# Performance work log

Measured on AMD Instinct MI355X. Metric: run time of the kernel, lower is better.

## Reference

```python
import jax, jax.numpy as jnp
import numpy as np

DT = 0.1
DISC = 5  # discretization: time grid arange(0, DT, DT/DISC) -> DISC-1 steps of h=DT/DISC


def setup_inputs() -> dict:
    key = jax.random.key(0)
    ks = jax.random.split(key, 16)
    B, T, D, Z, H = 32, 256, 128, 64, 256
    s = 0.08
    return {
        "x": jax.random.normal(ks[0], (B, T, D), dtype=jnp.float32),
        "h0": jnp.zeros((2, 1, Z), dtype=jnp.float32),
        "Wih0": jax.random.normal(ks[1], (Z, D), dtype=jnp.float32) * s,
        "Whh0": jax.random.normal(ks[2], (Z, Z), dtype=jnp.float32) * s,
        "bih0": jax.random.normal(ks[3], (Z,), dtype=jnp.float32) * s,
        "bhh0": jax.random.normal(ks[4], (Z,), dtype=jnp.float32) * s,
        "Wih1": jax.random.normal(ks[5], (Z, Z), dtype=jnp.float32) * s,
        "Whh1": jax.random.normal(ks[6], (Z, Z), dtype=jnp.float32) * s,
        "bih1": jax.random.normal(ks[7], (Z,), dtype=jnp.float32) * s,
        "bhh1": jax.random.normal(ks[8], (Z,), dtype=jnp.float32) * s,
        "Wh0": jax.random.normal(ks[9], (H, Z), dtype=jnp.float32) * s,
        "bh0": jax.random.normal(ks[10], (H,), dtype=jnp.float32) * s,
        "Wh1": jax.random.normal(ks[11], (H, H), dtype=jnp.float32) * s,
        "bh1": jax.random.normal(ks[12], (H,), dtype=jnp.float32) * s,
        "Wout": jax.random.normal(ks[13], (1, H), dtype=jnp.float32) * s,
        "bout": jax.random.normal(ks[14], (1,), dtype=jnp.float32) * s,
        "seq_len": 256,
    }


def _rnn_layer(xs, h_init, Wih, Whh, bih, bhh):
    # xs: (T, B, in) -> (T, B, Z); tanh RNN (nn.RNN, nonlinearity='tanh')
    def step(h, xt):
        h = jnp.tanh(xt @ Wih.T + bih + h @ Whh.T + bhh)
        return h, h
    _, ys = jax.lax.scan(step, h_init, xs)
    return ys


def _forward(x, h0, Wih0, Whh0, bih0, bhh0, Wih1, Whh1, bih1, bhh1,
             Wh0, bh0, Wh1, bh1, Wout, bout, seq_len):
    B, T, Z = x.shape[0], seq_len, h0.shape[-1]
    # reverse_sequences with full-length sequences == flip along time
    xr = jnp.flip(x, axis=1).transpose(1, 0, 2)  # (T, B, D)
    h0b = jnp.broadcast_to(h0, (2, B, Z))
    y0 = _rnn_layer(xr, h0b[0], Wih0, Whh0, bih0, bhh0)
    y1 = _rnn_layer(y0, h0b[1], Wih1, Whh1, bih1, bhh1)
    rnn_out = jnp.flip(y1.transpose(1, 0, 2), axis=1)  # (B, T, Z), pad_and_reverse

    # Hamiltonian MLP H(z): z_dim -> hidden -> hidden -> 1 (latent_func uses autograd.grad of H)
    def hamiltonian_sum(z):
        h = jnp.tanh(z @ Wh0.T + bh0)
        h = jnp.tanh(h @ Wh1.T + bh1)
        return (h @ Wout.T + bout).sum()
    grad_h = jax.grad(hamiltonian_sum)  # per-sample grads since H is per-sample

    # Yoshida 4th-order symplectic coefficients
    cbrt2 = 2.0 ** (1.0 / 3.0)
    w1 = 1.0 / (2.0 - cbrt2)
    w0 = -cbrt2 * w1
    cs = (w1 / 2.0, (w0 + w1) / 2.0, (w0 + w1) / 2.0, w1 / 2.0)
    ds = (w1, w0, w1)
    h_step = DT / DISC

    def yoshida_step(z, _):
        q, p = jnp.split(z, 2, axis=-1)
        for i in range(4):
            dHq, dHp = jnp.split(grad_h(jnp.concatenate([q, p], -1)), 2, -1)
            q = q + cs[i] * h_step * dHp  # drift: dq/dt = dH/dp
            if i < 3:
                dHq, dHp = jnp.split(grad_h(jnp.concatenate([q, p], -1)), 2, -1)
                p = p - ds[i] * h_step * dHq  # kick: dp/dt = -dH/dq
        return jnp.concatenate([q, p], -1), None

    # ode_output[:, t] = odeint(rnn_out[:, t+1]) for t < T-1; all independent -> batch them
    z0 = rnn_out[:, 1:, :].reshape(B * (T - 1), 2 * (Z // 2))
    zT, _ = jax.lax.scan(yoshida_step, z0, None, length=DISC - 1)
    ode = zT.reshape(B, T - 1, Z)
    return jnp.concatenate([ode, rnn_out[:, -1:, :]], axis=1)  # (B, T, Z)


def reference(x, h0, Wih0, Whh0, bih0, bhh0, Wih1, Whh1, bih1, bhh1,
              Wh0, bh0, Wh1, bh1, Wout, bout, seq_len):
    return _forward(x, h0, Wih0, Whh0, bih0, bhh0, Wih1, Whh1, bih1, bhh1,
                    Wh0, bh0, Wh1, bh1, Wout, bout, seq_len)
```

## Files before the change

kernel.cpp:

```cpp
#include <hip/hip_runtime.h>
#include <math.h>

#define T_LEN 256
#define B_SZ  32
#define ZD    64
#define HD    256
#define NSAMP (B_SZ*(T_LEN-1))
#define MBLK  32

typedef unsigned short u16;
typedef __attribute__((ext_vector_type(8))) _Float16 h8v;
typedef __attribute__((ext_vector_type(2))) _Float16 h2v;
typedef __attribute__((ext_vector_type(8))) unsigned short us8v;
typedef __attribute__((ext_vector_type(4))) float  f4v;

#define SZ_ZB   (B_SZ*(T_LEN-1)*ZD)
#define SZ_P0   ((T_LEN-1)*B_SZ*ZD)
#define OFF_ZB  0
#define OFF_P0  (OFF_ZB + SZ_ZB)
#define PK_WB  0
#define PK_WC  65536
#define PK_WA  131072
#define PK_WD  147456

__device__ __forceinline__ u16 f2h(float x) {
    _Float16 h = (_Float16)x;
    return __builtin_bit_cast(u16, h);
}
__device__ __forceinline__ float fast_tanh(float x) {
    float xc = fminf(fmaxf(x, -18.f), 18.f);
    float e2 = __builtin_amdgcn_exp2f(xc * 2.8853900817779268f);
    return (e2 - 1.f) * __builtin_amdgcn_rcpf(e2 + 1.f);
}
__device__ __forceinline__ f4v mfma16h(h8v a, h8v b, f4v c) {
    return __builtin_amdgcn_mfma_f32_16x16x32_f16(a, b, c, 0, 0, 0);
}
__device__ __forceinline__ h8v lds_frag(const u16* buf, int byt) {
    return *(const h8v*)((const char*)buf + byt);
}
__device__ __forceinline__ void store_h(u16* buf, int byt, float v) {
    *(u16*)((char*)buf + byt) = f2h(v);
}
__device__ __forceinline__ void barrier_lds() {
    asm volatile("s_waitcnt lgkmcnt(0)\n\ts_barrier" ::: "memory");
}

__device__ __forceinline__ h2v bch2(unsigned u) { return __builtin_bit_cast(h2v, u); }
__device__ __forceinline__ unsigned packh2(float a, float b) {
    h2v v; v[0] = (_Float16)a; v[1] = (_Float16)b;
    return __builtin_bit_cast(unsigned, v);
}
#if __has_builtin(__builtin_amdgcn_fdot2)
__device__ __forceinline__ float fdot2f(unsigned a, unsigned b, float c) {
    return __builtin_amdgcn_fdot2(bch2(a), bch2(b), c, false);
}
#else
__device__ __forceinline__ float fdot2f(unsigned a, unsigned b, float c) {
    h2v x = bch2(a), y = bch2(b);
    return c + (float)x[0] * (float)y[0] + (float)x[1] * (float)y[1];
}
#endif

__device__ __constant__ float c_coef[7] = {
     0.013512071919596578f,
    -0.027024143839193156f,
    -0.003512071919596575f,
     0.034048287678386313f,
    -0.003512071919596575f,
    -0.027024143839193156f,
     0.013512071919596578f
};

__global__ __launch_bounds__(256) void prep_pack(
    const float* __restrict__ Wh1, const float* __restrict__ Wh0, u16* __restrict__ pk)
{
    int i = blockIdx.x * 256 + threadIdx.x;
    u16 h = f2h(Wh1[i]);
    {
        int n = i >> 8, k = i & 255;
        int idx = ((((n >> 4) * 8 + (k >> 5)) * 64) + ((k >> 3) & 3) * 16 + (n & 15)) * 8 + (k & 7);
        pk[PK_WB + idx] = h;
    }
    {
        int k = i >> 8, n = i & 255;
        int idx = ((((n >> 4) * 8 + (k >> 5)) * 64) + ((k >> 3) & 3) * 16 + (n & 15)) * 8 + (k & 7);
        pk[PK_WC + idx] = h;
    }
    if (i < HD * ZD) {
        u16 h0 = f2h(Wh0[i]);
        {
            int n = i >> 6, k = i & 63;
            int idx = ((((n >> 4) * 2 + (k >> 5)) * 64) + ((k >> 3) & 3) * 16 + (n & 15)) * 8 + (k & 7);
            pk[PK_WA + idx] = h0;
        }
        {
            int k = i >> 6, n = i & 63;
            int idx = ((((n >> 4) * 8 + (k >> 5)) * 64) + ((k >> 3) & 3) * 16 + (n & 15)) * 8 + (k & 7);
            pk[PK_WD + idx] = h0;
        }
    }
}

__global__ __launch_bounds__(256) void p0_kernel(
    const float* __restrict__ x, const float* __restrict__ Wih0,
    const float* __restrict__ bih0, const float* __restrict__ bhh0,
    float* __restrict__ P0)
{
    __shared__ float xs[B_SZ * 128];
    int s = blockIdx.x;
    int t = (T_LEN - 1) - s;
    int tid = threadIdx.x;
#pragma unroll
    for (int p = 0; p < 4; ++p) {
        int idx4 = tid + p * 256;
        int b = idx4 >> 5;
        int k = (idx4 & 31) * 4;
        *(float4*)&xs[b * 128 + k] = *(const float4*)&x[b * (T_LEN * 128) + t * 128 + k];
    }
    int j = tid & 63, bq = tid >> 6;
    float wr[128];
#pragma unroll
    for (int k4 = 0; k4 < 32; ++k4) {
        float4 v = *(const float4*)&Wih0[j * 128 + k4 * 4];
        wr[k4*4+0]=v.x; wr[k4*4+1]=v.y; wr[k4*4+2]=v.z; wr[k4*4+3]=v.w;
    }
    float bias = bih0[j] + bhh0[j];
    __syncthreads();
    for (int p = 0; p < 8; ++p) {
        int b = bq * 8 + p;
        float a0 = bias, a1 = 0.f;
#pragma unroll
        for (int k4 = 0; k4 < 32; ++k4) {
            float4 v = *(const float4*)&xs[b * 128 + k4 * 4];
            a0 += v.x * wr[k4*4+0] + v.y * wr[k4*4+1];
            a1 += v.z * wr[k4*4+2] + v.w * wr[k4*4+3];
        }
        P0[(s * B_SZ + b) * ZD + j] = a0 + a1;
    }
}

__global__ __launch_bounds__(128, 1) void rnn_kernel(
    const float* __restrict__ P0, const float* __restrict__ h0in,
    const float* __restrict__ Whh0, const float* __restrict__ Wih1,
    const float* __restrict__ Whh1, const float* __restrict__ bih1,
    const float* __restrict__ bhh1,
    float* __restrict__ zbuf, float* __restrict__ out)
{
    __shared__ __align__(16) u16 h0buf[2][ZD];
    __shared__ __align__(16) u16 h1buf[2][ZD];
    const int b = blockIdx.x;
    const int tid = threadIdx.x;
    const int w = tid >> 6, j = tid & 63;

    unsigned wa[32], wb[32];
    float bias1 = 0.f;
    if (w == 0) {
#pragma unroll
        for (int q = 0; q < 16; ++q) {
            float4 v = *(const float4*)&Whh0[j * 64 + q * 4];
            wa[q*2+0] = packh2(v.x, v.y);
            wa[q*2+1] = packh2(v.z, v.w);
        }
        h0buf[0][j] = f2h(h0in[j]);
    } else {
#pragma unroll
        for (int q = 0; q < 16; ++q) {
            float4 v = *(const float4*)&Wih1[j * 64 + q * 4];
            wa[q*2+0] = packh2(v.x, v.y);
            wa[q*2+1] = packh2(v.z, v.w);
            float4 u = *(const float4*)&Whh1[j * 64 + q * 4];
            wb[q*2+0] = packh2(u.x, u.y);
            wb[q*2+1] = packh2(u.z, u.w);
        }
        bias1 = bih1[j] + bhh1[j];
        h1buf[0][j] = f2h(h0in[ZD + j]);
    }
    float a_cur = 0.f, a_nxt = 0.f;
    if (w == 0) {
        a_cur = P0[(0 * B_SZ + b) * ZD + j];
        a_nxt = P0[(1 * B_SZ + b) * ZD + j];
    }
    __syncthreads();

    for (int t = 0; t < T_LEN; ++t) {
        if (w == 0) {
            if (t < T_LEN - 1) {
                float a_new = (t + 2 < T_LEN - 1) ? P0[((t + 2) * B_SZ + b) * ZD + j] : 0.f;
                const u16* hp = h0buf[t & 1];
                float c0 = a_cur, c1 = 0.f, c2 = 0.f, c3 = 0.f;
#pragma unroll
                for (int pp = 0; pp < 8; ++pp) {
                    uint4 ha = *(const uint4*)(hp + pp * 8);
                    c0 = fdot2f(wa[pp*4+0], ha.x, c0);
                    c1 = fdot2f(wa[pp*4+1], ha.y, c1);
                    c2 = fdot2f(wa[pp*4+2], ha.z, c2);
                    c3 = fdot2f(wa[pp*4+3], ha.w, c3);
                }
                float y = fast_tanh((c0 + c1) + (c2 + c3));
                h0buf[(t & 1) ^ 1][j] = f2h(y);
                a_cur = a_nxt; a_nxt = a_new;
            }
        } else {
            if (t >= 1) {
                const u16* hp = h0buf[t & 1];
                const u16* gp = h1buf[(t + 1) & 1];
                float c0 = bias1, c1 = 0.f, c2 = 0.f, c3 = 0.f;
                float d0 = 0.f, d1 = 0.f, d2 = 0.f, d3 = 0.f;
#pragma unroll
                for (int pp = 0; pp < 8; ++pp) {
                    uint4 ha = *(const uint4*)(hp + pp * 8);
                    uint4 ga = *(const uint4*)(gp + pp * 8);
                    c0 = fdot2f(wa[pp*4+0], ha.x, c0);
                    c1 = fdot2f(wa[pp*4+1], ha.y, c1);
                    c2 = fdot2f(wa[pp*4+2], ha.z, c2);
                    c3 = fdot2f(wa[pp*4+3], ha.w, c3);
                    d0 = fdot2f(wb[pp*4+0], ga.x, d0);
                    d1 = fdot2f(wb[pp*4+1], ga.y, d1);
                    d2 = fdot2f(wb[pp*4+2], ga.z, d2);
                    d3 = fdot2f(wb[pp*4+3], ga.w, d3);
                }
                float y = fast_tanh(((c0 + c1) + (c2 + c3)) + ((d0 + d1) + (d2 + d3)));
                h1buf[t & 1][j] = f2h(y);
                int s = t - 1;
                int tau = (T_LEN - 2) - s;
                zbuf[(b * (T_LEN - 1) + tau) * ZD + j] = y;
                if (s == 0)
                    out[(b * T_LEN + (T_LEN - 1)) * ZD + j] = y;
            }
        }
        barrier_lds();
    }
}

__global__ __launch_bounds__(512, 1) void ode_kernel(
    const float* __restrict__ zbuf,
    const float* __restrict__ bh0, const float* __restrict__ bh1,
    const float* __restrict__ Wout, const u16* __restrict__ pk,
    float* __restrict__ out)
{
    __shared__ __align__(16) u16 sWA[16384];
    __shared__ __align__(16) u16 sWD[16384];
    __shared__ __align__(16) u16 aA[32 * 256];
    __shared__ __align__(16) u16 aB[32 * 256];
    __shared__ __align__(16) u16 zh[32 * 64];
    __shared__ __align__(16) float zq[32 * 64];

    const int tid  = threadIdx.x;
    const int w    = tid >> 6, lane = tid & 63;
    const int l15  = lane & 15, lg = lane >> 4;
    const int base = blockIdx.x * MBLK;

    h8v regWB[2][8], regWC[2][8];
    {
        const h8v* pWB = (const h8v*)(pk + PK_WB);
        const h8v* pWC = (const h8v*)(pk + PK_WC);
#pragma unroll
        for (int t = 0; t < 2; ++t)
#pragma unroll
            for (int ks = 0; ks < 8; ++ks) {
                int fi = ((w * 2 + t) * 8 + ks) * 64 + lane;
                regWB[t][ks] = pWB[fi];
                regWC[t][ks] = pWC[fi];
            }
    }
    {
        const us8v* gA = (const us8v*)(pk + PK_WA);
        const us8v* gD = (const us8v*)(pk + PK_WD);
#pragma unroll
        for (int r = 0; r < 4; ++r) {
            int idx = tid + r * 512;
            ((us8v*)sWA)[idx] = gA[idx];
            ((us8v*)sWD)[idx] = gD[idx];
        }
    }

    float bh0v[2], bh1v[2], wov[2];
#pragma unroll
    for (int t = 0; t < 2; ++t) {
        int col = (w * 2 + t) * 16 + l15;
        bh0v[t] = bh0[col]; bh1v[t] = bh1[col]; wov[t] = Wout[col];
    }

    {
        int m = tid >> 4, c4 = tid & 15;
        float4 v = *(const float4*)&zbuf[(size_t)(base + m) * ZD + c4 * 4];
        *(float4*)&zq[m * 64 + c4 * 4] = v;
        ushort4 hh;
        hh.x = f2h(v.x); hh.y = f2h(v.y); hh.z = f2h(v.z); hh.w = f2h(v.w);
        int byt = (m * 128 + c4 * 8) ^ ((m & 7) << 4);
        *(ushort4*)((char*)zh + byt) = hh;
    }
    __syncthreads();

#pragma unroll 1
    for (int e = 0; e < 28; ++e) {
        int ei = e % 7;
        f4v acc[2][2];
#pragma unroll
        for (int mt = 0; mt < 2; ++mt)
#pragma unroll
            for (int t = 0; t < 2; ++t) acc[mt][t] = f4v{0.f, 0.f, 0.f, 0.f};

#pragma unroll
        for (int ks = 0; ks < 2; ++ks) {
            h8v az[2];
#pragma unroll
            for (int mt = 0; mt < 2; ++mt) {
                int byt = ((mt * 16 + l15) * 128 + ks * 64 + lg * 16) ^ ((l15 & 7) << 4);
                az[mt] = lds_frag(zh, byt);
            }
#pragma unroll
            for (int t = 0; t < 2; ++t) {
                h8v bw = lds_frag(sWA, (((w * 2 + t) * 2 + ks) * 64 + lane) * 16);
#pragma unroll
                for (int mt = 0; mt < 2; ++mt)
                    acc[mt][t] = mfma16h(az[mt], bw, acc[mt][t]);
            }
        }
        float h0reg[2][2][4];
#pragma unroll
        for (int mt = 0; mt < 2; ++mt)
#pragma unroll
            for (int t = 0; t < 2; ++t)
#pragma unroll
                for (int r = 0; r < 4; ++r) {
                    float tv = fast_tanh(acc[mt][t][r] + bh0v[t]);
                    h0reg[mt][t][r] = tv;
                    int row = mt * 16 + lg * 4 + r;
                    int col = (w * 2 + t) * 16 + l15;
                    store_h(aA, (row * 512 + col * 2) ^ ((row & 7) << 4), tv);
                }
        __syncthreads();

#pragma unroll
        for (int mt = 0; mt < 2; ++mt)
#pragma unroll
            for (int t = 0; t < 2; ++t) acc[mt][t] = f4v{0.f, 0.f, 0.f, 0.f};
#pragma unroll
        for (int ks = 0; ks < 8; ++ks) {
            h8v ah[2];
#pragma unroll
            for (int mt = 0; mt < 2; ++mt) {
                int byt = ((mt * 16 + l15) * 512 + ks * 64 + lg * 16) ^ ((l15 & 7) << 4);
                ah[mt] = lds_frag(aA, byt);
            }
#pragma unroll
            for (int t = 0; t < 2; ++t)
#pragma unroll
                for (int mt = 0; mt < 2; ++mt)
                    acc[mt][t] = mfma16h(ah[mt], regWB[t][ks], acc[mt][t]);
        }
#pragma unroll
        for (int mt = 0; mt < 2; ++mt)
#pragma unroll
            for (int t = 0; t < 2; ++t)
#pragma unroll
                for (int r = 0; r < 4; ++r) {
                    float tv = fast_tanh(acc[mt][t][r] + bh1v[t]);
                    float g = wov[t] * (1.f - tv * tv);
                    int row = mt * 16 + lg * 4 + r;
                    int col = (w * 2 + t) * 16 + l15;
                    store_h(aB, (row * 512 + col * 2) ^ ((row & 7) << 4), g);
                }
        __syncthreads();

#pragma unroll
        for (int mt = 0; mt < 2; ++mt)
#pragma unroll
            for (int t = 0; t < 2; ++t) acc[mt][t] = f4v{0.f, 0.f, 0.f, 0.f};
#pragma unroll
        for (int ks = 0; ks < 8; ++ks) {
            h8v ah[2];
#pragma unroll
            for (int mt = 0; mt < 2; ++mt) {
                int byt = ((mt * 16 + l15) * 512 + ks * 64 + lg * 16) ^ ((l15 & 7) << 4);
                ah[mt] = lds_frag(aB, byt);
            }
#pragma unroll
            for (int t = 0; t < 2; ++t)
#pragma unroll
                for (int mt = 0; mt < 2; ++mt)
                    acc[mt][t] = mfma16h(ah[mt], regWC[t][ks], acc[mt][t]);
        }
#pragma unroll
        for (int mt = 0; mt < 2; ++mt)
#pragma unroll
            for (int t = 0; t < 2; ++t)
#pragma unroll
                for (int r = 0; r < 4; ++r) {
                    float hv = h0reg[mt][t][r];
                    float u = acc[mt][t][r] * (1.f - hv * hv);
                    int row = mt * 16 + lg * 4 + r;
                    int col = (w * 2 + t) * 16 + l15;
                    store_h(aA, (row * 512 + col * 2) ^ ((row & 7) << 4), u);
                }
        __syncthreads();

        if (w >= 4) {
            int nt = w - 4;
            f4v accd[2];
            accd[0] = f4v{0.f, 0.f, 0.f, 0.f};
            accd[1] = f4v{0.f, 0.f, 0.f, 0.f};
#pragma unroll
            for (int ks = 0; ks < 8; ++ks) {
                h8v ah[2];
#pragma unroll
                for (int mt = 0; mt < 2; ++mt) {
                    int byt = ((mt * 16 + l15) * 512 + ks * 64 + lg * 16) ^ ((l15 & 7) << 4);
                    ah[mt] = lds_frag(aA, byt);
                }
                h8v bw = lds_frag(sWD, ((nt * 8 + ks) * 64 + lane) * 16);
#pragma unroll
                for (int mt = 0; mt < 2; ++mt)
                    accd[mt] = mfma16h(ah[mt], bw, accd[mt]);
            }
            float cf = c_coef[ei];
            int col = nt * 16 + l15;
            bool drift = (ei & 1) == 0;
            bool active = drift ? (col >= 32) : (col < 32);
            int dcol = drift ? (col - 32) : (col + 32);
            if (active) {
#pragma unroll
                for (int mt = 0; mt < 2; ++mt)
#pragma unroll
                    for (int r = 0; r < 4; ++r) {
                        int row = mt * 16 + lg * 4 + r;
                        float nz = zq[row * 64 + dcol] + cf * accd[mt][r];
                        zq[row * 64 + dcol] = nz;
                        store_h(zh, (row * 128 + dcol * 2) ^ ((row & 7) << 4), nz);
                    }
            }
        }
        __syncthreads();
    }

    {
        int m = tid >> 4, c4 = tid & 15;
        int sidx = base + m;
        int b = sidx / 255;
        int tau = sidx - b * 255;
        float4 v = *(const float4*)&zq[m * 64 + c4 * 4];
        *(float4*)&out[((size_t)(b * T_LEN + tau)) * ZD + c4 * 4] = v;
    }
}

extern "C" void kernel_launch(void* const* d_in, const int* in_sizes, int n_in,
                              void* d_out, int out_size, void* d_ws, size_t ws_size,
                              hipStream_t stream)
{
    (void)in_sizes; (void)n_in; (void)out_size; (void)ws_size;
    const float* x    = (const float*)d_in[0];
    const float* h0in = (const float*)d_in[1];
    const float* Wih0 = (const float*)d_in[2];
    const float* Whh0 = (const float*)d_in[3];
    const float* bih0 = (const float*)d_in[4];
    const float* bhh0 = (const float*)d_in[5];
    const float* Wih1 = (const float*)d_in[6];
    const float* Whh1 = (const float*)d_in[7];
    const float* bih1 = (const float*)d_in[8];
    const float* bhh1 = (const float*)d_in[9];
    const float* Wh0  = (const float*)d_in[10];
    const float* bh0  = (const float*)d_in[11];
    const float* Wh1  = (const float*)d_in[12];
    const float* bh1  = (const float*)d_in[13];
    const float* Wout = (const float*)d_in[14];

    float* ws = (float*)d_ws;
    float* zb = ws + OFF_ZB;
    float* P0 = ws + OFF_P0;
    u16*   pk = (u16*)(ws + OFF_P0);
    float* out = (float*)d_out;

    p0_kernel<<<T_LEN - 1, 256, 0, stream>>>(x, Wih0, bih0, bhh0, P0);
    rnn_kernel<<<B_SZ, 128, 0, stream>>>(P0, h0in, Whh0, Wih1, Whh1, bih1, bhh1, zb, out);
    prep_pack<<<256, 256, 0, stream>>>(Wh1, Wh0, pk);
    ode_kernel<<<NSAMP / MBLK, 512, 0, stream>>>(zb, bh0, bh1, Wout, pk, out);
}
```

Before: 234.3 us.

## Halve ODE block rows and stream WB/WC weights from global each stage

Reduces the ODE kernel's per-block sample tile from 32 to 16 rows, doubling the grid so more blocks spread across compute units. To shrink LDS and register use, WA moves from LDS into registers, and a single weight register array is reloaded from global memory (L2) alternately with WB and WC each stage instead of keeping both resident. The aim is more parallelism and a smaller per-block footprint. In exchange each MFMA does less work per weight fragment, and every Euler substep adds repeated global weight loads that may stall the MFMA chains.

Measured after the change: 249.1 us. 6.3% more time.

```diff
diff --git a/kernel.cpp b/kernel.cpp
--- a/kernel.cpp
+++ b/kernel.cpp
@@ -6,7 +6,7 @@
 #define ZD    64
 #define HD    256
 #define NSAMP (B_SZ*(T_LEN-1))
-#define MBLK  32
+#define MBLK  16
 
 typedef unsigned short u16;
 typedef __attribute__((ext_vector_type(8))) _Float16 h8v;
@@ -238,38 +238,38 @@
     const float* __restrict__ Wout, const u16* __restrict__ pk,
     float* __restrict__ out)
 {
-    __shared__ __align__(16) u16 sWA[16384];
     __shared__ __align__(16) u16 sWD[16384];
-    __shared__ __align__(16) u16 aA[32 * 256];
-    __shared__ __align__(16) u16 aB[32 * 256];
-    __shared__ __align__(16) u16 zh[32 * 64];
-    __shared__ __align__(16) float zq[32 * 64];
+    __shared__ __align__(16) u16 aA[MBLK * 256];
+    __shared__ __align__(16) u16 aB[MBLK * 256];
+    __shared__ __align__(16) u16 zh[MBLK * 64];
+    __shared__ __align__(16) float zq[MBLK * 64];
 
     const int tid  = threadIdx.x;
     const int w    = tid >> 6, lane = tid & 63;
     const int l15  = lane & 15, lg = lane >> 4;
     const int base = blockIdx.x * MBLK;
 
-    h8v regWB[2][8], regWC[2][8];
+    const h8v* pWB = (const h8v*)(pk + PK_WB);
+    const h8v* pWC = (const h8v*)(pk + PK_WC);
+    const h8v* pWA = (const h8v*)(pk + PK_WA);
+
+    h8v regWA[2][2], wgt[2][8];
+#pragma unroll
+    for (int t = 0; t < 2; ++t)
+#pragma unroll
+        for (int ks = 0; ks < 2; ++ks)
+            regWA[t][ks] = pWA[((w * 2 + t) * 2 + ks) * 64 + lane];
+#pragma unroll
+    for (int t = 0; t < 2; ++t)
+#pragma unroll
+        for (int ks = 0; ks < 8; ++ks)
+            wgt[t][ks] = pWB[((w * 2 + t) * 8 + ks) * 64 + lane];
+
     {
-        const h8v* pWB = (const h8v*)(pk + PK_WB);
-        const h8v* pWC = (const h8v*)(pk + PK_WC);
-#pragma unroll
-        for (int t = 0; t < 2; ++t)
-#pragma unroll
-            for (int ks = 0; ks < 8; ++ks) {
-                int fi = ((w * 2 + t) * 8 + ks) * 64 + lane;
-                regWB[t][ks] = pWB[fi];
-                regWC[t][ks] = pWC[fi];
-            }
-    }
-    {
-        const us8v* gA = (const us8v*)(pk + PK_WA);
         const us8v* gD = (const us8v*)(pk + PK_WD);
 #pragma unroll
         for (int r = 0; r < 4; ++r) {
             int idx = tid + r * 512;
-            ((us8v*)sWA)[idx] = gA[idx];
             ((us8v*)sWD)[idx] = gD[idx];
         }
     }
@@ -281,7 +281,7 @@
         bh0v[t] = bh0[col]; bh1v[t] = bh1[col]; wov[t] = Wout[col];
     }
 
-    {
+    if (tid < 256) {
         int m = tid >> 4, c4 = tid & 15;
         float4 v = *(const float4*)&zbuf[(size_t)(base + m) * ZD + c4 * 4];
         *(float4*)&zq[m * 64 + c4 * 4] = v;
@@ -295,146 +295,110 @@
 #pragma unroll 1
     for (int e = 0; e < 28; ++e) {
         int ei = e % 7;
-        f4v acc[2][2];
-#pragma unroll
-        for (int mt = 0; mt < 2; ++mt)
-#pragma unroll
-            for (int t = 0; t < 2; ++t) acc[mt][t] = f4v{0.f, 0.f, 0.f, 0.f};
+        f4v acc[2];
+        acc[0] = f4v{0.f, 0.f, 0.f, 0.f};
+        acc[1] = f4v{0.f, 0.f, 0.f, 0.f};
 
 #pragma unroll
         for (int ks = 0; ks < 2; ++ks) {
-            h8v az[2];
-#pragma unroll
-            for (int mt = 0; mt < 2; ++mt) {
-                int byt = ((mt * 16 + l15) * 128 + ks * 64 + lg * 16) ^ ((l15 & 7) << 4);
-                az[mt] = lds_frag(zh, byt);
-            }
-#pragma unroll
-            for (int t = 0; t < 2; ++t) {
-                h8v bw = lds_frag(sWA, (((w * 2 + t) * 2 + ks) * 64 + lane) * 16);
-#pragma unroll
-                for (int mt = 0; mt < 2; ++mt)
-                    acc[mt][t] = mfma16h(az[mt], bw, acc[mt][t]);
-            }
-        }
-        float h0reg[2][2][4];
-#pragma unroll
-        for (int mt = 0; mt < 2; ++mt)
+            h8v az = lds_frag(zh, (l15 * 128 + ks * 64 + lg * 16) ^ ((l15 & 7) << 4));
 #pragma unroll
             for (int t = 0; t < 2; ++t)
-#pragma unroll
-                for (int r = 0; r < 4; ++r) {
-                    float tv = fast_tanh(acc[mt][t][r] + bh0v[t]);
-                    h0reg[mt][t][r] = tv;
-                    int row = mt * 16 + lg * 4 + r;
-                    int col = (w * 2 + t) * 16 + l15;
-                    store_h(aA, (row * 512 + col * 2) ^ ((row & 7) << 4), tv);
-                }
+                acc[t] = mfma16h(az, regWA[t][ks], acc[t]);
+        }
+        float h0reg[2][4];
+#pragma unroll
+        for (int t = 0; t < 2; ++t)
+#pragma unroll
+            for (int r = 0; r < 4; ++r) {
+                float tv = fast_tanh(acc[t][r] + bh0v[t]);
+                h0reg[t][r] = tv;
+                int row = lg * 4 + r;
+                int col = (w * 2 + t) * 16 + l15;
+                store_h(aA, (row * 512 + col * 2) ^ ((row & 7) << 4), tv);
+            }
         __syncthreads();
 
-#pragma unroll
-        for (int mt = 0; mt < 2; ++mt)
-#pragma unroll
-            for (int t = 0; t < 2; ++t) acc[mt][t] = f4v{0.f, 0.f, 0.f, 0.f};
+        acc[0] = f4v{0.f, 0.f, 0.f, 0.f};
+        acc[1] = f4v{0.f, 0.f, 0.f, 0.f};
 #pragma unroll
         for (int ks = 0; ks < 8; ++ks) {
-            h8v ah[2];
-#pragma unroll
-            for (int mt = 0; mt < 2; ++mt) {
-                int byt = ((mt * 16 + l15) * 512 + ks * 64 + lg * 16) ^ ((l15 & 7) << 4);
-                ah[mt] = lds_frag(aA, byt);
-            }
+            h8v ah = lds_frag(aA, (l15 * 512 + ks * 64 + lg * 16) ^ ((l15 & 7) << 4));
 #pragma unroll
             for (int t = 0; t < 2; ++t)
-#pragma unroll
-                for (int mt = 0; mt < 2; ++mt)
-                    acc[mt][t] = mfma16h(ah[mt], regWB[t][ks], acc[mt][t]);
-        }
-#pragma unroll
-        for (int mt = 0; mt < 2; ++mt)
+                acc[t] = mfma16h(ah, wgt[t][ks], acc[t]);
+        }
+#pragma unroll
+        for (int t = 0; t < 2; ++t)
+#pragma unroll
+            for (int r = 0; r < 4; ++r) {
+                float tv = fast_tanh(acc[t][r] + bh1v[t]);
+                float g = wov[t] * (1.f - tv * tv);
+                int row = lg * 4 + r;
+                int col = (w * 2 + t) * 16 + l15;
+                store_h(aB, (row * 512 + col * 2) ^ ((row & 7) << 4), g);
+            }
+#pragma unroll
+        for (int t = 0; t < 2; ++t)
+#pragma unroll
+            for (int ks = 0; ks < 8; ++ks)
+                wgt[t][ks] = pWC[((w * 2 + t) * 8 + ks) * 64 + lane];
+        __syncthreads();
+
+        acc[0] = f4v{0.f, 0.f, 0.f, 0.f};
+        acc[1] = f4v{0.f, 0.f, 0.f, 0.f};
+#pragma unroll
+        for (int ks = 0; ks < 8; ++ks) {
+            h8v ah = lds_frag(aB, (l15 * 512 + ks * 64 + lg * 16) ^ ((l15 & 7) << 4));
 #pragma unroll
             for (int t = 0; t < 2; ++t)
-#pragma unroll
-                for (int r = 0; r < 4; ++r) {
-                    float tv = fast_tanh(acc[mt][t][r] + bh1v[t]);
-                    float g = wov[t] * (1.f - tv * tv);
-                    int row = mt * 16 + lg * 4 + r;
-                    int col = (w * 2 + t) * 16 + l15;
-                    store_h(aB, (row * 512 + col * 2) ^ ((row & 7) << 4), g);
-                }
-        __syncthreads();
-
-#pragma unroll
-        for (int mt = 0; mt < 2; ++mt)
-#pragma unroll
-            for (int t = 0; t < 2; ++t) acc[mt][t] = f4v{0.f, 0.f, 0.f, 0.f};
-#pragma unroll
-        for (int ks = 0; ks < 8; ++ks) {
-            h8v ah[2];
-#pragma unroll
-            for (int mt = 0; mt < 2; ++mt) {
-                int byt = ((mt * 16 + l15) * 512 + ks * 64 + lg * 16) ^ ((l15 & 7) << 4);
-                ah[mt] = lds_frag(aB, byt);
-            }
-#pragma unroll
-            for (int t = 0; t < 2; ++t)
-#pragma unroll
-                for (int mt = 0; mt < 2; ++mt)
-                    acc[mt][t] = mfma16h(ah[mt], regWC[t][ks], acc[mt][t]);
-        }
-#pragma unroll
-        for (int mt = 0; mt < 2; ++mt)
-#pragma unroll
-            for (int t = 0; t < 2; ++t)
-#pragma unroll
-                for (int r = 0; r < 4; ++r) {
-                    float hv = h0reg[mt][t][r];
-                    float u = acc[mt][t][r] * (1.f - hv * hv);
-                    int row = mt * 16 + lg * 4 + r;
-                    int col = (w * 2 + t) * 16 + l15;
-                    store_h(aA, (row * 512 + col * 2) ^ ((row & 7) << 4), u);
-                }
+                acc[t] = mfma16h(ah, wgt[t][ks], acc[t]);
+        }
+#pragma unroll
+        for (int t = 0; t < 2; ++t)
+#pragma unroll
+            for (int r = 0; r < 4; ++r) {
+                float hv = h0reg[t][r];
+                float u = acc[t][r] * (1.f - hv * hv);
+                int row = lg * 4 + r;
+                int col = (w * 2 + t) * 16 + l15;
+                store_h(aA, (row * 512 + col * 2) ^ ((row & 7) << 4), u);
+            }
+#pragma unroll
+        for (int t = 0; t < 2; ++t)
+#pragma unroll
+            for (int ks = 0; ks < 8; ++ks)
+                wgt[t][ks] = pWB[((w * 2 + t) * 8 + ks) * 64 + lane];
         __syncthreads();
 
         if (w >= 4) {
             int nt = w - 4;
-            f4v accd[2];
-            accd[0] = f4v{0.f, 0.f, 0.f, 0.f};
-            accd[1] = f4v{0.f, 0.f, 0.f, 0.f};
+            f4v accd = f4v{0.f, 0.f, 0.f, 0.f};
 #pragma unroll
             for (int ks = 0; ks < 8; ++ks) {
-                h8v ah[2];
-#pragma unroll
-                for (int mt = 0; mt < 2; ++mt) {
-                    int byt = ((mt * 16 + l15) * 512 + ks * 64 + lg * 16) ^ ((l15 & 7) << 4);
-                    ah[mt] = lds_frag(aA, byt);
+                h8v ah = lds_frag(aA, (l15 * 512 + ks * 64 + lg * 16) ^ ((l15 & 7) << 4));
+                h8v bw = lds_frag(sWD, ((nt * 8 + ks) * 64 + lane) * 16);
+                accd = mfma16h(ah, bw, accd);
+            }
+            float cf = c_coef[ei];
+            int dc = nt * 16 + l15;
+            bool drift = (ei & 1) == 0;
+            bool active = drift ? (dc >= 32) : (dc < 32);
+            int dcol = drift ? (dc - 32) : (dc + 32);
+            if (active) {
+#pragma unroll
+                for (int r = 0; r < 4; ++r) {
+                    int row = lg * 4 + r;
+                    float nz = zq[row * 64 + dcol] + cf * accd[r];
+                    zq[row * 64 + dcol] = nz;
+                    store_h(zh, (row * 128 + dcol * 2) ^ ((row & 7) << 4), nz);
                 }
-                h8v bw = lds_frag(sWD, ((nt * 8 + ks) * 64 + lane) * 16);
-#pragma unroll
-                for (int mt = 0; mt < 2; ++mt)
-                    accd[mt] = mfma16h(ah[mt], bw, accd[mt]);
-            }
-            float cf = c_coef[ei];
-            int col = nt * 16 + l15;
-            bool drift = (ei & 1) == 0;
-            bool active = drift ? (col >= 32) : (col < 32);
-            int dcol = drift ? (col - 32) : (col + 32);
-            if (active) {
-#pragma unroll
-                for (int mt = 0; mt < 2; ++mt)
-#pragma unroll
-                    for (int r = 0; r < 4; ++r) {
-                        int row = mt * 16 + lg * 4 + r;
-                        float nz = zq[row * 64 + dcol] + cf * accd[mt][r];
-                        zq[row * 64 + dcol] = nz;
-                        store_h(zh, (row * 128 + dcol * 2) ^ ((row & 7) << 4), nz);
-                    }
             }
         }
         __syncthreads();
     }
 
-    {
+    if (tid < 256) {
         int m = tid >> 4, c4 = tid & 15;
         int sidx = base + m;
         int b = sidx / 255;
```
